# Optimization experiments

Measured on AMD Instinct MI355X. Metric: run time of the kernel, lower is better.

## Reference

```python
import jax, jax.numpy as jnp
import numpy as np

B, S, HID = 2, 2048, 2048
H, D_NOPE, D_ROPE = 16, 128, 64
KV_LORA = 192            # forced so v_head dim == pad_hd == 128 (see torch view)
NUM_SLOTS, MAX_LEN = 8, 2048
SCALE = D_NOPE ** -0.5


def setup_inputs() -> dict:
    key = jax.random.key(0)
    ks = jax.random.split(key, 4)
    return {
        "hidden_states": jax.random.normal(ks[0], (B, S, HID), jnp.float32),
        "Wq": jax.random.normal(ks[1], (H * (D_NOPE + D_ROPE), HID), jnp.float32) * 0.02,
        "Wkv": jax.random.normal(ks[2], (KV_LORA + D_ROPE, HID), jnp.float32) * 0.02,
        "Wo": jax.random.normal(ks[3], (HID, H * D_NOPE), jnp.float32) * 0.02,
        "k_cache": jnp.zeros((NUM_SLOTS, MAX_LEN, 1, D_NOPE), jnp.float32),
        "v_cache": jnp.zeros((NUM_SLOTS, MAX_LEN, 1, D_NOPE), jnp.float32),
        "slot_mapping": jnp.arange(B, dtype=jnp.int32),
        "kv_start_indices": jnp.zeros((B,), jnp.int32),
        "seq_lens": jnp.full((B,), S, jnp.int32),
        "positions": jnp.arange(S, dtype=jnp.int32),
    }


def reference(hidden_states, Wq, Wkv, Wo, k_cache, v_cache,
              slot_mapping, kv_start_indices, seq_lens, positions):
    # q / low-rank kv projections (nn.Linear convention: x @ W.T)
    q = (hidden_states @ Wq.T).reshape(B, S, H, D_NOPE + D_ROPE)
    q_nope = q[..., :D_NOPE]                       # [B,S,H,128]
    kv = hidden_states @ Wkv.T                     # [B,S,256]
    k = kv[..., :D_NOPE][:, :, None, :]            # [B,S,1,128] single latent kv head
    v = kv[..., D_NOPE:][:, :, None, :]            # [B,S,1,128]

    # paged KV-cache scatter (prefill: kv_start_indices == 0, write [0:S))
    k_cache = k_cache.at[slot_mapping, :S].set(k)
    v_cache = v_cache.at[slot_mapping, :S].set(v)

    # gather history back (max_l = seq_lens.max() == S at prefill, static)
    k_hist = k_cache[slot_mapping, :S]             # [B,L,1,128]
    v_hist = v_cache[slot_mapping, :S]

    # MQA attention: sum over singleton kv-head axis == repeat_interleave broadcast
    scores = jnp.einsum('bshd,blod->bhsl', q_nope, k_hist) * SCALE  # [B,H,S,L]
    causal = jnp.triu(jnp.ones((S, S), bool), k=1)  # diagonal = start(0)+1
    scores = jnp.where(causal[None, None], -jnp.inf, scores)
    attn = jax.nn.softmax(scores, axis=-1)
    out = jnp.einsum('bhsl,blod->bshd', attn, v_hist)  # [B,S,H,128]
    out = out.reshape(B, S, H * D_NOPE)
    return out @ Wo.T
```

## Files before the change

kernel.cpp:

```cpp
#include <hip/hip_runtime.h>
#include <hip/hip_bf16.h>
#include <stdint.h>


typedef __attribute__((ext_vector_type(4))) float f32x4;
typedef __attribute__((ext_vector_type(8))) short bf16x8;
typedef __attribute__((ext_vector_type(4))) short bf16x4;

__device__ __forceinline__ unsigned short f2bf(float f) {
    union { float f; unsigned u; } v; v.f = f;
    unsigned u = v.u;
    return (unsigned short)((u + 0x7fffu + ((u >> 16) & 1u)) >> 16);
}

__device__ __forceinline__ short bf_rn(float f) {
    __hip_bfloat16 h = __float2bfloat16(f);
    short s; __builtin_memcpy(&s, &h, 2); return s;
}

__device__ __forceinline__ float exp2_raw(float x) {
#if __has_builtin(__builtin_amdgcn_exp2f)
    return __builtin_amdgcn_exp2f(x);
#else
    return exp2f(x);
#endif
}

#define MFMA32(a,b,c) __builtin_amdgcn_mfma_f32_16x16x32_bf16((a),(b),(c),0,0,0)
#if defined(__HIP_DEVICE_COMPILE__)
#define MFMA16(a,b,c) __builtin_amdgcn_mfma_f32_16x16x16bf16_1k((a),(b),(c),0,0,0)
#else
#define MFMA16(a,b,c) (c)
#endif

#define GLD_LDS16(g,l) __builtin_amdgcn_global_load_lds( \
    (const __attribute__((address_space(1))) unsigned int*)(g), \
    (__attribute__((address_space(3))) unsigned int*)(l), 16, 0, 0)

__global__ void cvt_all(const float* __restrict__ in, unsigned short* __restrict__ out, int n4) {
    const int stride = gridDim.x * blockDim.x;
    for (int i = blockIdx.x * blockDim.x + threadIdx.x; i < n4; i += stride) {
        float4 v = ((const float4*)in)[i];
        ushort4 r;
        r.x = f2bf(v.x); r.y = f2bf(v.y); r.z = f2bf(v.z); r.w = f2bf(v.w);
        ((ushort4*)out)[i] = r;
    }
}

__global__ void cvt_wqkv(const float* __restrict__ wq, const float* __restrict__ wkv,
                         unsigned short* __restrict__ out) {
    const int row = blockIdx.x;
    const bool isq = (row < 2048);
    const float sc = isq ? 0.1275174331181861f : 1.0f;
    const float* srcp = isq ? (wq + (long)((row >> 7) * 192 + (row & 127)) * 2048)
                            : (wkv + (long)(row - 2048) * 2048);
    const float4* ip = (const float4*)srcp;
    ushort4* op = (ushort4*)(out + (long)row * 2048);
    for (int i = threadIdx.x; i < 512; i += 256) {
        float4 v = ip[i];
        ushort4 r;
        r.x = f2bf(v.x * sc); r.y = f2bf(v.y * sc);
        r.z = f2bf(v.z * sc); r.w = f2bf(v.w * sc);
        op[i] = r;
    }
}

__global__ void transpose_v(const unsigned short* __restrict__ qkv, unsigned short* __restrict__ vt) {
    __shared__ unsigned short tile[32][33];
    const int b = blockIdx.z, dt = blockIdx.y, st = blockIdx.x;
    const int x = threadIdx.x, y = threadIdx.y;
    const int s0 = st * 32, d0 = dt * 32;
    #pragma unroll
    for (int i = 0; i < 4; ++i)
        tile[y + i * 8][x] = qkv[((long)(b * 2048 + s0 + y + i * 8)) * 2304 + 2176 + d0 + x];
    __syncthreads();
    #pragma unroll
    for (int i = 0; i < 4; ++i)
        vt[((long)(b * 128 + d0 + y + i * 8)) * 2048 + s0 + x] = tile[x][y + i * 8];
}

template<int OUT_BF16>
__global__ __launch_bounds__(256, 2)
void gemm_bt(const unsigned short* __restrict__ A,
             const unsigned short* __restrict__ B,
             void* __restrict__ Cp, int M, int N, int K) {
    __shared__ unsigned short As[128 * 64];
    __shared__ unsigned short Bs[128 * 64];
    const int t = threadIdx.x;
    const int wave = t >> 6, lane = t & 63;
    const int wr = wave >> 1, wc = wave & 1;
    const int l15 = lane & 15, l4 = lane >> 4;

    const int nbx = gridDim.x;
    const int nwg = nbx * gridDim.y;
    const int borig = blockIdx.y * nbx + blockIdx.x;
    const int bswz = (borig & 7) * (nwg >> 3) + (borig >> 3);
    const long m0 = (bswz / nbx) * 128L, n0 = (bswz % nbx) * 128L;

    const unsigned short* asrc[4];
    const unsigned short* bsrc[4];
    #pragma unroll
    for (int it = 0; it < 4; ++it) {
        const int c = it * 4 + wave;
        const int row = c * 8 + (lane >> 3);
        const int gsw = (lane & 7) ^ (row & 7);
        asrc[it] = A + (m0 + row) * K + gsw * 8;
        bsrc[it] = B + (n0 + row) * K + gsw * 8;
    }

    f32x4 acc[4][4] = {};
    for (int k0 = 0; k0 < K; k0 += 64) {
        #pragma unroll
        for (int it = 0; it < 4; ++it) {
            const int c = it * 4 + wave;
            GLD_LDS16(asrc[it] + k0, As + c * 512);
            GLD_LDS16(bsrc[it] + k0, Bs + c * 512);
        }
        __syncthreads();
        #pragma unroll
        for (int ks = 0; ks < 2; ++ks) {
            bf16x8 af[4], bfr[4];
            #pragma unroll
            for (int m = 0; m < 4; ++m) {
                const int row = wr * 64 + m * 16 + l15;
                const int slot = (ks * 4 + l4) ^ (row & 7);
                af[m] = *(const bf16x8*)(As + row * 64 + slot * 8);
            }
            #pragma unroll
            for (int n = 0; n < 4; ++n) {
                const int row = wc * 64 + n * 16 + l15;
                const int slot = (ks * 4 + l4) ^ (row & 7);
                bfr[n] = *(const bf16x8*)(Bs + row * 64 + slot * 8);
            }
            #pragma unroll
            for (int m = 0; m < 4; ++m)
                #pragma unroll
                for (int n = 0; n < 4; ++n)
                    acc[m][n] = MFMA32(af[m], bfr[n], acc[m][n]);
        }
        __syncthreads();
    }

    #pragma unroll
    for (int m = 0; m < 4; ++m)
        #pragma unroll
        for (int n = 0; n < 4; ++n) {
            const long rg = m0 + wr * 64 + m * 16 + l4 * 4;
            const long cg = n0 + wc * 64 + n * 16 + l15;
            #pragma unroll
            for (int i = 0; i < 4; ++i) {
                float v = acc[m][n][i];
                if (OUT_BF16) ((unsigned short*)Cp)[(rg + i) * N + cg] = f2bf(v);
                else          ((float*)Cp)[(rg + i) * N + cg] = v;
            }
        }
}

__global__ __launch_bounds__(256, 2)
void attn_fused(const unsigned short* __restrict__ QKV,
                const unsigned short* __restrict__ VT,
                unsigned short* __restrict__ AO) {
    __shared__ unsigned short Ks[2][64 * 128];
    __shared__ unsigned short Vs[2][128 * 64];
    const int t = threadIdx.x;
    const int wave = t >> 6, lane = t & 63;
    const int l15 = lane & 15, l4 = lane >> 4;
    const int bid = blockIdx.x;
    const int p = bid >> 4;
    const int hgb = bid & 15;
    const int hg = hgb >> 1, b = hgb & 1;
    const int h = hg * 2 + (wave >> 1);
    const int qsub = wave & 1;
    const long rowB = (long)b * 2048;

    const unsigned short* ksrc[4];
    const unsigned short* vsrc[4];
    #pragma unroll
    for (int it = 0; it < 4; ++it) {
        const int c = it * 4 + wave;
        const int krow = c * 4 + (lane >> 4);
        const int ksp = (lane & 15) ^ (krow & 15);
        ksrc[it] = QKV + (rowB + krow) * 2304 + 2048 + ksp * 8;
        const int vd = c * 8 + (lane >> 3);
        const int vsp = (lane & 7) ^ (vd & 7);
        vsrc[it] = VT + ((long)b * 128 + vd) * 2048 + vsp * 8;
    }

#define STAGE(bufi, jj0) do { \
    _Pragma("unroll") \
    for (int it = 0; it < 4; ++it) { \
        const int c = it * 4 + wave; \
        GLD_LDS16(ksrc[it] + (long)(jj0) * 2304, &Ks[bufi][c * 512]); \
        GLD_LDS16(vsrc[it] + (jj0), &Vs[bufi][c * 512]); \
    } \
} while (0)

    for (int ph = 0; ph < 2; ++ph) {
        const int qt = ph ? p : (63 - p);
        const int q0 = qt * 32;
        const int q0w = q0 + qsub * 16;
        const int nt = (qt >> 1) + 1;

        bf16x8 qf[4];
        {
            const unsigned short* qp = QKV + (rowB + q0w + l15) * 2304 + h * 128;
            #pragma unroll
            for (int kb = 0; kb < 4; ++kb)
                qf[kb] = *(const bf16x8*)(qp + kb * 32 + l4 * 8);
        }

        f32x4 o[8] = {};
        float lsum = 0.f;

        STAGE(0, 0);
        int cur = 0;

        for (int tt = 0; tt < nt; ++tt) {
            const int j0 = tt * 64;
            asm volatile("s_waitcnt vmcnt(0)" ::: "memory");
            __builtin_amdgcn_s_barrier();
            if (tt + 1 < nt) STAGE(cur ^ 1, j0 + 64);

            const unsigned short* ksBase = cur ? &Ks[1][0] : &Ks[0][0];
            f32x4 st[4];
            __builtin_amdgcn_s_setprio(1);
            #pragma unroll
            for (int jkv = 0; jkv < 4; ++jkv) {
                const unsigned short* krp = ksBase + (jkv * 16 + l15) * 128;
                f32x4 s0 = {};
                #pragma unroll
                for (int kb = 0; kb < 4; ++kb) {
                    const int slot = (kb * 4 + l4) ^ l15;
                    bf16x8 kf = *(const bf16x8*)(krp + slot * 8);
                    s0 = MFMA32(kf, qf[kb], s0);
                }
                st[jkv] = s0;
            }
            __builtin_amdgcn_s_setprio(0);

            if (tt + 1 == nt) {
                const int qrow = q0w + l15;
                #pragma unroll
                for (int jkv = 0; jkv < 4; ++jkv)
                    #pragma unroll
                    for (int i = 0; i < 4; ++i) {
                        const int kpos = j0 + jkv * 16 + l4 * 4 + i;
                        if (kpos > qrow) st[jkv][i] = -3.0e38f;
                    }
            }
            float ps = 0.f;
            bf16x4 pa[4];
            #pragma unroll
            for (int jkv = 0; jkv < 4; ++jkv) {
                float p0 = exp2_raw(st[jkv][0]);
                float p1 = exp2_raw(st[jkv][1]);
                float p2 = exp2_raw(st[jkv][2]);
                float p3 = exp2_raw(st[jkv][3]);
                ps += (p0 + p1) + (p2 + p3);
#if defined(__HIP_DEVICE_COMPILE__)
                unsigned r0, r1;
                asm("v_cvt_pk_bf16_f32 %0, %1, %2" : "=v"(r0) : "v"(p0), "v"(p1));
                asm("v_cvt_pk_bf16_f32 %0, %1, %2" : "=v"(r1) : "v"(p2), "v"(p3));
                union { unsigned u[2]; bf16x4 v; } cvt;
                cvt.u[0] = r0; cvt.u[1] = r1;
                pa[jkv] = cvt.v;
#else
                bf16x4 v = { bf_rn(p0), bf_rn(p1), bf_rn(p2), bf_rn(p3) };
                pa[jkv] = v;
#endif
            }
            lsum += ps;

            const unsigned short* vsBase = cur ? &Vs[1][0] : &Vs[0][0];
            __builtin_amdgcn_s_setprio(1);
            #pragma unroll
            for (int dj = 0; dj < 8; ++dj) {
                const int d = dj * 16 + l15;
                const unsigned short* vrow = vsBase + d * 64;
                const int dsw = (d & 7) << 3;
                #pragma unroll
                for (int jkv = 0; jkv < 4; ++jkv) {
                    bf16x4 vf = *(const bf16x4*)(vrow + ((jkv * 16 + l4 * 4) ^ dsw));
                    o[dj] = MFMA16(pa[jkv], vf, o[dj]);
                }
            }
            __builtin_amdgcn_s_setprio(0);
            cur ^= 1;
        }

        float lrow = lsum;
        lrow += __shfl_xor(lrow, 16);
        lrow += __shfl_xor(lrow, 32);
        float il[4];
        #pragma unroll
        for (int i = 0; i < 4; ++i)
            il[i] = 1.0f / __shfl(lrow, l4 * 4 + i);
        #pragma unroll
        for (int dj = 0; dj < 8; ++dj)
            #pragma unroll
            for (int i = 0; i < 4; ++i) {
                const long qrow = rowB + q0w + l4 * 4 + i;
                AO[qrow * 2048 + h * 128 + dj * 16 + l15] = (unsigned short)bf_rn(o[dj][i] * il[i]);
            }
        __syncthreads();
    }
#undef STAGE
}

extern "C" void kernel_launch(void* const* d_in, const int* in_sizes, int n_in,
                              void* d_out, int out_size, void* d_ws, size_t ws_size,
                              hipStream_t stream) {
    const float* hs  = (const float*)d_in[0];
    const float* Wq  = (const float*)d_in[1];
    const float* Wkv = (const float*)d_in[2];
    const float* Wo  = (const float*)d_in[3];
    char* ws = (char*)d_ws;
    unsigned short* h_bf   = (unsigned short*)(ws + 0);
    unsigned short* wqkv_bf= (unsigned short*)(ws + 16777216);
    unsigned short* wo_bf  = (unsigned short*)(ws + 26214400);
    unsigned short* qkv_bf = (unsigned short*)(ws + 34603008);
    unsigned short* vt_bf  = (unsigned short*)(ws + 53477376);
    unsigned short* ao_bf  = (unsigned short*)(ws + 54525952);
    float* out = (float*)d_out;

    cvt_all <<<2048, 256, 0, stream>>>(hs, h_bf, 2097152);
    cvt_all <<<2048, 256, 0, stream>>>(Wo, wo_bf, 1048576);
    cvt_wqkv<<<2304, 256, 0, stream>>>(Wq, Wkv, wqkv_bf);

    gemm_bt<1><<<dim3(18, 32), 256, 0, stream>>>(h_bf, wqkv_bf, qkv_bf, 4096, 2304, 2048);
    transpose_v<<<dim3(64, 4, 2), dim3(32, 8), 0, stream>>>(qkv_bf, vt_bf);
    attn_fused<<<dim3(512, 1, 1), 256, 0, stream>>>(qkv_bf, vt_bf, ao_bf);
    gemm_bt<0><<<dim3(16, 32), 256, 0, stream>>>(ao_bf, wo_bf, out, 4096, 2048, 2048);
}
```

Measured before the change: 167.7 us.

## Single-buffer V tile in attention to allow three blocks per CU

The V tile in shared memory becomes single-buffered, cutting the attention kernel's LDS use so that launch bounds can ask for three resident blocks per CU. K stays double-buffered and is prefetched at the start of each iteration. The next V tile is loaded only after the PV MFMAs finish, with extra waitcnt and barrier points around it. The trade-off is that V load latency is now less hidden and there is one more barrier per tile. The tighter register budget from the higher launch bound may also cause spills.

```diff
diff --git a/kernel.cpp b/kernel.cpp
--- a/kernel.cpp
+++ b/kernel.cpp
@@ -156,12 +156,12 @@
         }
 }
 
-__global__ __launch_bounds__(256, 2)
+__global__ __launch_bounds__(256, 3)
 void attn_fused(const unsigned short* __restrict__ QKV,
                 const unsigned short* __restrict__ VT,
                 unsigned short* __restrict__ AO) {
     __shared__ unsigned short Ks[2][64 * 128];
-    __shared__ unsigned short Vs[2][128 * 64];
+    __shared__ unsigned short Vs[128 * 64];
     const int t = threadIdx.x;
     const int wave = t >> 6, lane = t & 63;
     const int l15 = lane & 15, l4 = lane >> 4;
@@ -186,12 +186,19 @@
         vsrc[it] = VT + ((long)b * 128 + vd) * 2048 + vsp * 8;
     }
 
-#define STAGE(bufi, jj0) do { \
+#define STAGE_K(bufi, jj0) do { \
     _Pragma("unroll") \
     for (int it = 0; it < 4; ++it) { \
         const int c = it * 4 + wave; \
         GLD_LDS16(ksrc[it] + (long)(jj0) * 2304, &Ks[bufi][c * 512]); \
-        GLD_LDS16(vsrc[it] + (jj0), &Vs[bufi][c * 512]); \
+    } \
+} while (0)
+
+#define STAGE_V(jj0) do { \
+    _Pragma("unroll") \
+    for (int it = 0; it < 4; ++it) { \
+        const int c = it * 4 + wave; \
+        GLD_LDS16(vsrc[it] + (jj0), &Vs[c * 512]); \
     } \
 } while (0)
 
@@ -212,14 +219,16 @@
         f32x4 o[8] = {};
         float lsum = 0.f;
 
-        STAGE(0, 0);
+        STAGE_K(0, 0);
+        STAGE_V(0);
+        asm volatile("s_waitcnt vmcnt(0)" ::: "memory");
+        __builtin_amdgcn_s_barrier();
         int cur = 0;
 
         for (int tt = 0; tt < nt; ++tt) {
             const int j0 = tt * 64;
-            asm volatile("s_waitcnt vmcnt(0)" ::: "memory");
-            __builtin_amdgcn_s_barrier();
-            if (tt + 1 < nt) STAGE(cur ^ 1, j0 + 64);
+            const bool pf = (tt + 1 < nt);
+            if (pf) STAGE_K(cur ^ 1, j0 + 64);
 
             const unsigned short* ksBase = cur ? &Ks[1][0] : &Ks[0][0];
             f32x4 st[4];
@@ -271,12 +280,15 @@
             }
             lsum += ps;
 
-            const unsigned short* vsBase = cur ? &Vs[1][0] : &Vs[0][0];
+            if (pf) asm volatile("s_waitcnt vmcnt(4)" ::: "memory");
+            else    asm volatile("s_waitcnt vmcnt(0)" ::: "memory");
+            __builtin_amdgcn_s_barrier();
+
             __builtin_amdgcn_s_setprio(1);
             #pragma unroll
             for (int dj = 0; dj < 8; ++dj) {
                 const int d = dj * 16 + l15;
-                const unsigned short* vrow = vsBase + d * 64;
+                const unsigned short* vrow = &Vs[d * 64];
                 const int dsw = (d & 7) << 3;
                 #pragma unroll
                 for (int jkv = 0; jkv < 4; ++jkv) {
@@ -285,6 +297,10 @@
                 }
             }
             __builtin_amdgcn_s_setprio(0);
+
+            asm volatile("s_waitcnt vmcnt(0)" ::: "memory");
+            __builtin_amdgcn_s_barrier();
+            if (pf) STAGE_V(j0 + 64);
             cur ^= 1;
         }
 
@@ -302,9 +318,11 @@
                 const long qrow = rowB + q0w + l4 * 4 + i;
                 AO[qrow * 2048 + h * 128 + dj * 16 + l15] = (unsigned short)bf_rn(o[dj][i] * il[i]);
             }
+        asm volatile("s_waitcnt vmcnt(0)" ::: "memory");
         __syncthreads();
     }
-#undef STAGE
+#undef STAGE_K
+#undef STAGE_V
 }
 
 extern "C" void kernel_launch(void* const* d_in, const int* in_sizes, int n_in,
```

Result: no change. 169.2 us (+0.9%).
